# Performance work log

Measured on AMD Instinct MI355X. Metric: run time of the kernel, lower is better.

## Reference

```python
import jax, jax.numpy as jnp
import numpy as np

B, L, C, S, W, R = 2, 32, 32, 64, 64, 32
MH = 32  # forcing MLP hidden


def _conv3d(x, w, b, pad_hw):
    # x: [B, Cin, L, S, W], w: [Cout, Cin, 1, kh, kw]
    y = jax.lax.conv_general_dilated(
        x, w, window_strides=(1, 1, 1),
        padding=[(0, 0), (pad_hw, pad_hw), (pad_hw, pad_hw)],
        dimension_numbers=('NCDHW', 'OIDHW', 'NCDHW'))
    return y + b[None, :, None, None, None]


def _forward(x, listT, params_log_base, dispersion_mod, fm_W1, fm_b1, fm_W2, fm_b2,
             forcing_scale, U_re, U_im, V_re, V_im, pW_re, pW_im, pb_re, pb_im,
             convr_w, convr_b, convi_w, convi_b, projc_w, projc_b, ln_w, ln_b):
    b, l, c, s, w = x.shape
    r = U_re.shape[-1]
    pad = s // 4
    dt = listT.reshape(b, l, 1, 1, 1)

    # FFT with mirror padding along S
    xp = jnp.pad(x, ((0, 0), (0, 0), (0, 0), (pad, pad), (0, 0)), mode='reflect')
    h = jnp.fft.fft2(xp.astype(jnp.complex64), axes=(-2, -1), norm='ortho')

    # complex channel projection
    proj_W = pW_re + 1j * pW_im
    h = jnp.einsum('blcsw,cd->bldsw', h, proj_W)
    h = h + (pb_re + 1j * pb_im)[None, None, :, None, None]

    # back to spatial, crop pad, re-FFT
    hs = jnp.fft.ifft2(h, axes=(-2, -1), norm='ortho')[..., pad:-pad, :]
    h = jnp.fft.fft2(hs, axes=(-2, -1), norm='ortho')

    U = U_re + 1j * U_im          # [C, S, R]
    V = V_re + 1j * V_im          # [C, W, R]
    # zq[b,l,c,r,q] = sum_{s,w} h * conj(U)[c,s,r] * V[c,w,q]
    zq = jnp.einsum('blcsw,csr,cwq->blcrq', h, jnp.conj(U), V)

    nu_base = jnp.exp(params_log_base[0] + dispersion_mod[0]).reshape(1, 1, c, r, 1)
    th_base = jnp.exp(params_log_base[1] + dispersion_mod[1]).reshape(1, 1, c, r, 1)

    # forcing modulation
    ctx = x.mean(axis=(-2, -1))                       # [B, L, C]
    inp = jnp.concatenate([ctx, dt.reshape(b, l, 1)], axis=-1)
    mid = jnp.tanh(inp @ fm_W1 + fm_b1)
    mod = (mid @ fm_W2 + fm_b2).reshape(b, l, c, r, 2)
    dnu = (forcing_scale * jnp.tanh(mod[..., 0]))[..., None]
    dth = (forcing_scale * jnp.tanh(mod[..., 1]))[..., None]

    nu_t = jnp.maximum(nu_base * dt + dnu, 1e-6)       # [B, L, C, R, 1]
    th_t = th_base * dt + dth
    lamb = jnp.exp(jax.lax.complex(-nu_t, th_t))       # complex [B, L, C, R, 1]

    gamma = jnp.sqrt(jnp.maximum(1.0 - jnp.exp(-2.0 * nu_t), 1e-12))
    x_in = zq * gamma.astype(zq.dtype)                 # [B, L, C, R, R]

    # parallel linear-recurrence scan: z_t = lamb_t * z_{t-1} + x_t
    def comb(a, bb):
        a1, x1 = a
        a2, x2 = bb
        return a1 * a2, a2 * x1 + x2
    _, z_out = jax.lax.associative_scan(comb, (lamb, x_in), axis=1)

    # reconstruct spectral field and inverse FFT
    h_rec = jnp.einsum('blcrq,cwq,csr->blcsw', z_out, jnp.conj(V), U)
    h_sp = jnp.fft.ifft2(h_rec, axes=(-2, -1), norm='ortho')

    xr = jnp.transpose(h_sp.real, (0, 2, 1, 3, 4))     # [B, C, L, S, W]
    xi = jnp.transpose(h_sp.imag, (0, 2, 1, 3, 4))
    hr = _conv3d(xr, convr_w, convr_b, 1)
    hi = _conv3d(xi, convi_w, convi_b, 1)
    hf = _conv3d(jnp.concatenate([hr, hi], axis=1), projc_w, projc_b, 0)
    hf = jnp.transpose(hf, (0, 2, 1, 3, 4))            # [B, L, C, S, W]

    # LayerNorm over [S, W]
    mu = hf.mean(axis=(-2, -1), keepdims=True)
    var = hf.var(axis=(-2, -1), keepdims=True)
    hf = (hf - mu) / jnp.sqrt(var + 1e-5) * ln_w + ln_b

    return x + hf


def setup_inputs() -> dict:
    key = jax.random.key(0)
    ks = jax.random.split(key, 20)
    f32 = jnp.float32
    x = jax.random.normal(ks[0], (B, L, C, S, W), dtype=f32)
    listT = jax.random.uniform(ks[1], (B, L), dtype=f32, minval=0.5, maxval=1.5)

    r_min, r_max = 0.8, 0.99
    u1 = jax.random.uniform(ks[2], (C, R), dtype=f32)
    u2 = jax.random.uniform(ks[3], (C, R), dtype=f32)
    nu_log = jnp.log(-0.5 * jnp.log(u1 * (r_max ** 2 - r_min ** 2) + r_min ** 2))
    theta_log = jnp.log(u2 * (2.0 * np.pi))
    params_log_base = jnp.stack([nu_log, theta_log], axis=0)
    dispersion_mod = jnp.zeros((2, C, R), dtype=f32)

    fm_W1 = jax.random.normal(ks[4], (C + 1, MH), dtype=f32) / np.sqrt(C + 1)
    fm_b1 = jnp.zeros((MH,), dtype=f32)
    fm_W2 = jax.random.normal(ks[5], (MH, C * R * 2), dtype=f32) / np.sqrt(MH)
    fm_b2 = jnp.zeros((C * R * 2,), dtype=f32)
    forcing_scale = jnp.float32(0.1)

    cplx_scale = 1.0 / np.sqrt(2.0)
    U_re = jax.random.normal(ks[6], (C, S, R), dtype=f32) * cplx_scale / np.sqrt(S)
    U_im = jax.random.normal(ks[7], (C, S, R), dtype=f32) * cplx_scale / np.sqrt(S)
    V_re = jax.random.normal(ks[8], (C, W, R), dtype=f32) * cplx_scale / np.sqrt(W)
    V_im = jax.random.normal(ks[9], (C, W, R), dtype=f32) * cplx_scale / np.sqrt(W)
    pW_re = jax.random.normal(ks[10], (C, C), dtype=f32) * cplx_scale / np.sqrt(C)
    pW_im = jax.random.normal(ks[11], (C, C), dtype=f32) * cplx_scale / np.sqrt(C)
    pb_re = jnp.zeros((C,), dtype=f32)
    pb_im = jnp.zeros((C,), dtype=f32)

    convr_w = jax.random.normal(ks[12], (C, C, 1, 3, 3), dtype=f32) * (1.0 / np.sqrt(C * 9))
    convr_b = jnp.zeros((C,), dtype=f32)
    convi_w = jax.random.normal(ks[13], (C, C, 1, 3, 3), dtype=f32) * (1.0 / np.sqrt(C * 9))
    convi_b = jnp.zeros((C,), dtype=f32)
    projc_w = jax.random.normal(ks[14], (C, 2 * C, 1, 1, 1), dtype=f32) * (1.0 / np.sqrt(2 * C))
    projc_b = jnp.zeros((C,), dtype=f32)

    ln_w = jnp.ones((S, W), dtype=f32)
    ln_b = jnp.zeros((S, W), dtype=f32)

    return dict(x=x, listT=listT, params_log_base=params_log_base,
                dispersion_mod=dispersion_mod, fm_W1=fm_W1, fm_b1=fm_b1,
                fm_W2=fm_W2, fm_b2=fm_b2, forcing_scale=forcing_scale,
                U_re=U_re, U_im=U_im, V_re=V_re, V_im=V_im,
                pW_re=pW_re, pW_im=pW_im, pb_re=pb_re, pb_im=pb_im,
                convr_w=convr_w, convr_b=convr_b, convi_w=convi_w, convi_b=convi_b,
                projc_w=projc_w, projc_b=projc_b, ln_w=ln_w, ln_b=ln_b)


def reference(x, listT, params_log_base, dispersion_mod, fm_W1, fm_b1, fm_W2, fm_b2,
              forcing_scale, U_re, U_im, V_re, V_im, pW_re, pW_im, pb_re, pb_im,
              convr_w, convr_b, convi_w, convi_b, projc_w, projc_b, ln_w, ln_b):
    return _forward(x, listT, params_log_base, dispersion_mod, fm_W1, fm_b1, fm_W2,
                    fm_b2, forcing_scale, U_re, U_im, V_re, V_im, pW_re, pW_im,
                    pb_re, pb_im, convr_w, convr_b, convi_w, convi_b, projc_w,
                    projc_b, ln_w, ln_b)
```

## Files before the change

### kernel.cpp

```cpp
#include <hip/hip_runtime.h>


typedef __attribute__((ext_vector_type(8))) short short8;
typedef __attribute__((ext_vector_type(4))) float floatx4;

__device__ __forceinline__ unsigned pack_bf16(float re, float im) {
  unsigned a = __float_as_uint(re), b = __float_as_uint(im);
  a = (a + 0x7FFFu + ((a >> 16) & 1u)) >> 16;
  b = (b + 0x7FFFu + ((b >> 16) & 1u)) >> 16;
  return a | (b << 16);
}
__device__ __forceinline__ unsigned short bf16r(float v) {
  unsigned a = __float_as_uint(v);
  return (unsigned short)((a + 0x7FFFu + ((a >> 16) & 1u)) >> 16);
}

__global__ __launch_bounds__(256) void k_mixprep(
    const float* __restrict__ x, const float* __restrict__ pWr,
    const float* __restrict__ pWi,
    const float* __restrict__ U_re, const float* __restrict__ U_im,
    const float* __restrict__ V_re, const float* __restrict__ V_im,
    const float* __restrict__ projc_w, const float* __restrict__ convr_w,
    const float* __restrict__ convi_w,
    unsigned* __restrict__ hs, float* __restrict__ ctxp,
    unsigned* __restrict__ zqA, unsigned* __restrict__ recA,
    unsigned* __restrict__ recB, unsigned* __restrict__ Wtb) {
  __shared__ __align__(16) char smem[33280];
  const int tid = threadIdx.x;
  if (blockIdx.x < 1024) {
    unsigned* xb_s = (unsigned*)smem;
    float(*red)[16][2] = (float(*)[16][2])(smem + 20480);
    unsigned* outb = (unsigned*)smem;
    const int bl = blockIdx.x >> 4;
    const int seg = blockIdx.x & 15;
    const int pxbase = seg * 256;
    const float* xb = x + (size_t)bl * 131072 + pxbase;
    float csa = 0.f, csb = 0.f;
#pragma unroll
    for (int t = 0; t < 4; ++t) {
      int i = t * 256 + tid;
      int c2 = i & 15, g4 = i >> 4;
      float4 a = *(const float4*)(xb + (2 * c2) * 4096 + g4 * 4);
      float4 b = *(const float4*)(xb + (2 * c2 + 1) * 4096 + g4 * 4);
      csa += a.x + a.y + a.z + a.w;
      csb += b.x + b.y + b.z + b.w;
#pragma unroll
      for (int j = 0; j < 4; ++j) {
        int px = g4 * 4 + j;
        xb_s[px * 20 + (((c2 >> 2) ^ (px & 3)) << 2) + (c2 & 3)] =
            pack_bf16(((const float*)&a)[j], ((const float*)&b)[j]);
      }
    }
    red[tid & 15][tid >> 4][0] = csa;
    red[tid & 15][tid >> 4][1] = csb;
    const int lane = tid & 63, wv = tid >> 6;
    const int qd = lane >> 4, ln = lane & 15;
    short8 arL, aiL, arH, aiH;
#pragma unroll
    for (int j = 0; j < 8; ++j) {
      int ci = qd * 8 + j;
      ((short*)&arL)[j] = (short)bf16r(pWr[ci * 32 + ln]);
      ((short*)&aiL)[j] = (short)bf16r(pWi[ci * 32 + ln]);
      ((short*)&arH)[j] = (short)bf16r(pWr[ci * 32 + 16 + ln]);
      ((short*)&aiH)[j] = (short)bf16r(pWi[ci * 32 + 16 + ln]);
    }
    __syncthreads();
    if (tid < 32) {
      int c2 = tid >> 1, part = tid & 1;
      float s = 0.f;
#pragma unroll
      for (int w = 0; w < 16; ++w) s += red[c2][w][part];
      ctxp[(bl * 16 + seg) * 32 + 2 * c2 + part] = s;
    }
    floatx4 RL[4], IL[4], RH[4], IH[4];
#pragma unroll
    for (int pt = 0; pt < 4; ++pt) {
      int pxt = wv * 4 + pt;
      int pxl = pxt * 16 + ln;
      short8 bfr = *(const short8*)&xb_s[pxl * 20 + ((qd ^ (pxl & 3)) << 2)];
      floatx4 z4 = {0.f, 0.f, 0.f, 0.f};
      RL[pt] = __builtin_amdgcn_mfma_f32_16x16x32_bf16(arL, bfr, z4, 0, 0, 0);
      IL[pt] = __builtin_amdgcn_mfma_f32_16x16x32_bf16(aiL, bfr, z4, 0, 0, 0);
      RH[pt] = __builtin_amdgcn_mfma_f32_16x16x32_bf16(arH, bfr, z4, 0, 0, 0);
      IH[pt] = __builtin_amdgcn_mfma_f32_16x16x32_bf16(aiH, bfr, z4, 0, 0, 0);
    }
    __syncthreads();
#pragma unroll
    for (int pt = 0; pt < 4; ++pt) {
      int px = (wv * 4 + pt) * 16 + ln;
#pragma unroll
      for (int j = 0; j < 4; ++j) {
        outb[(qd * 4 + j) * 260 + px] = pack_bf16(RL[pt][j], IL[pt][j]);
        outb[(16 + qd * 4 + j) * 260 + px] = pack_bf16(RH[pt][j], IH[pt][j]);
      }
    }
    __syncthreads();
    unsigned* ho = hs + (size_t)bl * 131072 + pxbase;
    const int px4 = tid & 63, dg = tid >> 6;
#pragma unroll
    for (int dd = 0; dd < 8; ++dd) {
      int d = dg * 8 + dd;
      uint4 v = *(const uint4*)&outb[d * 260 + px4 * 4];
      *(uint4*)(ho + d * 4096 + px4 * 4) = v;
    }
  } else if (blockIdx.x < 1088) {
    float2* A2 = (float2*)smem;
    float2* tw = (float2*)(smem + 16384);
    const int id = blockIdx.x - 1024;
    const int c = id >> 1, src = id & 1;
    const float* Ar = (src ? V_re : U_re) + c * 2048;
    const float* Ai = (src ? V_im : U_im) + c * 2048;
    if (tid < 64) {
      float sa, ca;
      sincosf((float)tid * 0.09817477042468103f, &sa, &ca);
      tw[tid] = make_float2(ca, sa);
    }
#pragma unroll
    for (int t = 0; t < 8; ++t) {
      int idx = t * 256 + tid;
      A2[idx] = make_float2(Ar[idx], Ai[idx]);
    }
    __syncthreads();
    const int kw = tid >> 2, mg = tid & 3;
    float sr[8] = {0.f, 0.f, 0.f, 0.f, 0.f, 0.f, 0.f, 0.f};
    float si[8] = {0.f, 0.f, 0.f, 0.f, 0.f, 0.f, 0.f, 0.f};
#pragma unroll 4
    for (int n = 0; n < 64; ++n) {
      float2 w = tw[(kw * n) & 63];
      float ws = src ? -w.y : w.y;
#pragma unroll
      for (int t4 = 0; t4 < 4; ++t4) {
        float4 p = *(const float4*)&A2[n * 32 + mg * 8 + t4 * 2];
        sr[2 * t4]     += p.x * w.x - p.y * ws;
        si[2 * t4]     += p.x * ws + p.y * w.x;
        sr[2 * t4 + 1] += p.z * w.x - p.w * ws;
        si[2 * t4 + 1] += p.z * ws + p.w * w.x;
      }
    }
#pragma unroll
    for (int j = 0; j < 8; ++j) {
      float r = sr[j] * 0.125f, i2 = si[j] * 0.125f;
      int m = mg * 8 + j;
      unsigned p_ri  = pack_bf16(r, i2);
      unsigned p_rmi = pack_bf16(r, -i2);
      unsigned p_ir  = pack_bf16(i2, r);
      unsigned p_mir = pack_bf16(-i2, r);
      if (src == 0) {
        zqA[((c * 4 + 2) * 32 + m) * 64 + kw] = p_ri;
        zqA[((c * 4 + 3) * 32 + m) * 64 + kw] = p_mir;
        recA[((c * 2 + 0) * 64 + kw) * 32 + m] = p_rmi;
        recA[((c * 2 + 1) * 64 + kw) * 32 + m] = p_ir;
      } else {
        zqA[((c * 4 + 0) * 32 + m) * 64 + kw] = p_rmi;
        zqA[((c * 4 + 1) * 32 + m) * 64 + kw] = p_ir;
        recB[((c * 2 + 0) * 64 + kw) * 32 + m] = p_ri;
        recB[((c * 2 + 1) * 64 + kw) * 32 + m] = p_mir;
      }
    }
  } else {
    int gid = (blockIdx.x - 1088) * 256 + tid;
    if (gid < 9216) {
      int co = gid / 288;
      int r2 = gid - co * 288;
      int tap = r2 >> 5, ci = r2 & 31;
      float sr = 0.f, si = 0.f;
      for (int m = 0; m < 32; ++m) {
        sr += projc_w[co * 64 + m]      * convr_w[(m * 32 + ci) * 9 + tap];
        si += projc_w[co * 64 + 32 + m] * convi_w[(m * 32 + ci) * 9 + tap];
      }
      Wtb[gid] = pack_bf16(sr, si);
    }
  }
}

__global__ __launch_bounds__(256) void k_zq(
    const unsigned* __restrict__ hs, const short* __restrict__ zqA,
    float2* __restrict__ zq,
    const float* __restrict__ ctxp, const float* __restrict__ listT,
    const float* __restrict__ plb, const float* __restrict__ dmod,
    const float* __restrict__ W1, const float* __restrict__ b1,
    const float* __restrict__ W2, const float* __restrict__ b2,
    const float* __restrict__ fscale,
    float2* __restrict__ lam, float* __restrict__ gam) {
  __shared__ unsigned HsB[4096];
  __shared__ unsigned T2[2048];
  __shared__ float mid_s[32];
  __shared__ float ctxs[32];
  const int tid = threadIdx.x;
  if (blockIdx.x >= 2048) {
    int bl = blockIdx.x - 2048;
    float dt = listT[bl];
    if (tid < 32) {
      float s = 0.f;
#pragma unroll
      for (int sg = 0; sg < 16; ++sg) s += ctxp[(bl * 16 + sg) * 32 + tid];
      ctxs[tid] = s * (1.f / 4096.f);
    }
    __syncthreads();
    if (tid < 32) {
      float a = b1[tid];
      for (int j = 0; j < 32; ++j) a += ctxs[j] * W1[j * 32 + tid];
      a += dt * W1[1024 + tid];
      mid_s[tid] = tanhf(a);
    }
    __syncthreads();
    float fs = fscale[0];
#pragma unroll
    for (int u = 0; u < 4; ++u) {
      int cr = u * 256 + tid;
      int col = cr * 2;
      float m0 = b2[col], m1 = b2[col + 1];
      for (int h = 0; h < 32; ++h) {
        float mh = mid_s[h];
        float2 w2 = *(const float2*)&W2[h * 2048 + col];
        m0 += mh * w2.x;
        m1 += mh * w2.y;
      }
      float dnu = fs * tanhf(m0);
      float dth = fs * tanhf(m1);
      float nub = expf(plb[cr] + dmod[cr]);
      float thb = expf(plb[1024 + cr] + dmod[1024 + cr]);
      float nut = fmaxf(nub * dt + dnu, 1e-6f);
      float tht = thb * dt + dth;
      float e = expf(-nut);
      float sa, ca;
      sincosf(tht, &sa, &ca);
      float g = sqrtf(fmaxf(1.f - expf(-2.f * nut), 1e-12f));
      int o = bl * 1024 + cr;
      lam[o] = make_float2(e * ca, e * sa);
      gam[o] = g;
    }
    return;
  }
  const int blc = blockIdx.x;
  const int c = blc & 31;
  const int lane = tid & 63, wv = tid >> 6;
  const int qd = lane >> 4, ln = lane & 15;
  const int mt = wv >> 1, nth = wv & 1;
  {
    const uint4* hp = (const uint4*)(hs + (size_t)blc * 4096);
#pragma unroll
    for (int it = 0; it < 4; ++it) {
      int i4 = tid + it * 256;
      uint4 v = hp[i4];
      int s = i4 >> 4, w4 = i4 & 15;
      *(uint4*)&HsB[s * 64 + ((w4 ^ (s & 15)) << 2)] = v;
    }
  }
  const short* zA = zqA + (size_t)c * 4 * 32 * 128;
  short8 a1[4], a2[4], a3[4], a4[4];
#pragma unroll
  for (int t = 0; t < 4; ++t) {
    int row = mt * 16 + ln;
    a1[t] = *(const short8*)(zA + (0 * 32 + row) * 128 + t * 32 + qd * 8);
    a2[t] = *(const short8*)(zA + (1 * 32 + row) * 128 + t * 32 + qd * 8);
    a3[t] = *(const short8*)(zA + (2 * 32 + row) * 128 + t * 32 + qd * 8);
    a4[t] = *(const short8*)(zA + (3 * 32 + row) * 128 + t * 32 + qd * 8);
  }
  __syncthreads();
#pragma unroll
  for (int nti = 0; nti < 2; ++nti) {
    int nt = nth * 2 + nti;
    int n = nt * 16 + ln;
    floatx4 accr = {0.f, 0.f, 0.f, 0.f}, acci = {0.f, 0.f, 0.f, 0.f};
#pragma unroll
    for (int t = 0; t < 4; ++t) {
      short8 b = *(const short8*)&HsB[n * 64 + (((4 * t + qd) ^ (n & 15)) << 2)];
      accr = __builtin_amdgcn_mfma_f32_16x16x32_bf16(a1[t], b, accr, 0, 0, 0);
      acci = __builtin_amdgcn_mfma_f32_16x16x32_bf16(a2[t], b, acci, 0, 0, 0);
    }
#pragma unroll
    for (int j = 0; j < 4; ++j) {
      int q = mt * 16 + qd * 4 + j;
      int s = n;
      T2[q * 64 + (((s >> 2) ^ (q & 15)) << 2) + (s & 3)] = pack_bf16(accr[j], acci[j]);
    }
  }
  __syncthreads();
  {
    const int mt2 = wv >> 1, nt2 = wv & 1;
    int n = nt2 * 16 + ln;
    floatx4 zr = {0.f, 0.f, 0.f, 0.f}, zi = {0.f, 0.f, 0.f, 0.f};
#pragma unroll
    for (int t = 0; t < 4; ++t) {
      short8 b = *(const short8*)&T2[n * 64 + (((4 * t + qd) ^ (n & 15)) << 2)];
      zr = __builtin_amdgcn_mfma_f32_16x16x32_bf16(a3[t], b, zr, 0, 0, 0);
      zi = __builtin_amdgcn_mfma_f32_16x16x32_bf16(a4[t], b, zi, 0, 0, 0);
    }
    float2* zo = zq + (size_t)blc * 1024;
#pragma unroll
    for (int j = 0; j < 4; ++j) {
      int r = mt2 * 16 + qd * 4 + j;
      zo[r * 32 + n] = make_float2(zr[j], zi[j]);
    }
  }
}

__global__ __launch_bounds__(256) void k_scan(const float2* __restrict__ lam,
                                              const float* __restrict__ gam,
                                              const float2* __restrict__ zin,
                                              unsigned* __restrict__ zsp,
                                              int zst) {
  __shared__ float2 se[4][64];
  __shared__ float2 pe[4][64];
  __shared__ float2 cr_s[4][64];
  const int bc = blockIdx.x >> 4;
  const int b = bc >> 5, c = bc & 31;
  const int rq0 = (blockIdx.x & 15) * 64;
  const int seg = threadIdx.x >> 6, u = threadIdx.x & 63;
  const int rq = rq0 + u, r = rq >> 5;
  const int t0 = seg * 8;
  float2 s = make_float2(0.f, 0.f), P = make_float2(1.f, 0.f);
  float2 zloc[8], Ps[8];
  float2 v = zin[((size_t)(b * 32 + t0) * 32 + c) * 1024 + rq];
  float2 lm = lam[(b * 32 + t0) * 1024 + c * 32 + r];
  float g = gam[(b * 32 + t0) * 1024 + c * 32 + r];
#pragma unroll
  for (int i = 0; i < 8; ++i) {
    float2 nv, nlm;
    float ng;
    if (i < 7) {
      int t = t0 + i + 1;
      nv = zin[((size_t)(b * 32 + t) * 32 + c) * 1024 + rq];
      nlm = lam[(b * 32 + t) * 1024 + c * 32 + r];
      ng = gam[(b * 32 + t) * 1024 + c * 32 + r];
    }
    float nr = lm.x * s.x - lm.y * s.y + g * v.x;
    float ni = lm.x * s.y + lm.y * s.x + g * v.y;
    s = make_float2(nr, ni);
    float pr = P.x * lm.x - P.y * lm.y;
    float pi = P.x * lm.y + P.y * lm.x;
    P = make_float2(pr, pi);
    zloc[i] = s;
    Ps[i] = P;
    v = nv; lm = nlm; g = ng;
  }
  se[seg][u] = s;
  pe[seg][u] = P;
  __syncthreads();
  if (threadIdx.x < 64) {
    float2 c1 = se[0][u];
    float2 p1 = pe[1][u], s1 = se[1][u];
    float2 c2 = make_float2(s1.x + p1.x * c1.x - p1.y * c1.y,
                            s1.y + p1.x * c1.y + p1.y * c1.x);
    float2 p2 = pe[2][u], s2 = se[2][u];
    float2 c3 = make_float2(s2.x + p2.x * c2.x - p2.y * c2.y,
                            s2.y + p2.x * c2.y + p2.y * c2.x);
    cr_s[0][u] = make_float2(0.f, 0.f);
    cr_s[1][u] = c1;
    cr_s[2][u] = c2;
    cr_s[3][u] = c3;
  }
  __syncthreads();
  float2 cr = cr_s[seg][u];
#pragma unroll
  for (int i = 0; i < 8; ++i) {
    float zr = zloc[i].x + Ps[i].x * cr.x - Ps[i].y * cr.y;
    float zi = zloc[i].y + Ps[i].x * cr.y + Ps[i].y * cr.x;
    size_t idx = ((size_t)(b * 32 + t0 + i) * 32 + c) * 1024 + rq;
    zsp[idx * zst] = pack_bf16(zr, zi);
  }
}

__global__ __launch_bounds__(256) void k_rec(const unsigned* __restrict__ zs,
                                             int zst,
                                             const short* __restrict__ recA,
                                             const short* __restrict__ recB,
                                             unsigned* __restrict__ hsp) {
  __shared__ unsigned zB[1024];
  __shared__ unsigned P[2048];
  const int blc = blockIdx.x;
  const int c = blc & 31;
  const int tid = threadIdx.x;
  const int lane = tid & 63, wv = tid >> 6;
  const int qd = lane >> 4, ln = lane & 15;
  {
    const unsigned* zp = zs + (size_t)blc * 1024 * zst;
#pragma unroll
    for (int it = 0; it < 4; ++it) {
      int i = tid + it * 256;
      unsigned pv = zp[(size_t)i * zst];
      int r = i >> 5, q = i & 31;
      zB[q * 32 + (((r >> 2) ^ (q & 7)) << 2) + (r & 3)] = pv;
    }
  }
  const short* rA = recA + (size_t)c * 2 * 64 * 64;
  short8 a5[2], a6[2];
#pragma unroll
  for (int t = 0; t < 2; ++t) {
    int row = wv * 16 + ln;
    a5[t] = *(const short8*)(rA + (0 * 64 + row) * 64 + t * 32 + qd * 8);
    a6[t] = *(const short8*)(rA + (1 * 64 + row) * 64 + t * 32 + qd * 8);
  }
  __syncthreads();
#pragma unroll
  for (int nt = 0; nt < 2; ++nt) {
    int n = nt * 16 + ln;
    floatx4 pr = {0.f, 0.f, 0.f, 0.f}, pi = {0.f, 0.f, 0.f, 0.f};
#pragma unroll
    for (int t = 0; t < 2; ++t) {
      short8 b = *(const short8*)&zB[n * 32 + (((4 * t + qd) ^ (n & 7)) << 2)];
      pr = __builtin_amdgcn_mfma_f32_16x16x32_bf16(a5[t], b, pr, 0, 0, 0);
      pi = __builtin_amdgcn_mfma_f32_16x16x32_bf16(a6[t], b, pi, 0, 0, 0);
    }
#pragma unroll
    for (int j = 0; j < 4; ++j) {
      int s = wv * 16 + qd * 4 + j;
      int q = n;
      P[s * 32 + (((q >> 2) ^ (s & 7)) << 2) + (q & 3)] = pack_bf16(pr[j], pi[j]);
    }
  }
  __syncthreads();
  const short* rB = recB + (size_t)c * 2 * 64 * 64;
  short8 pa[2];
#pragma unroll
  for (int t = 0; t < 2; ++t) {
    int row = wv * 16 + ln;
    pa[t] = *(const short8*)&P[row * 32 + (((4 * t + qd) ^ (row & 7)) << 2)];
  }
#pragma unroll
  for (int nt = 0; nt < 4; ++nt) {
    int n = nt * 16 + ln;
    floatx4 hr = {0.f, 0.f, 0.f, 0.f}, hi = {0.f, 0.f, 0.f, 0.f};
#pragma unroll
    for (int t = 0; t < 2; ++t) {
      short8 b5 = *(const short8*)(rB + (0 * 64 + n) * 64 + t * 32 + qd * 8);
      short8 b6 = *(const short8*)(rB + (1 * 64 + n) * 64 + t * 32 + qd * 8);
      hr = __builtin_amdgcn_mfma_f32_16x16x32_bf16(pa[t], b5, hr, 0, 0, 0);
      hi = __builtin_amdgcn_mfma_f32_16x16x32_bf16(pa[t], b6, hi, 0, 0, 0);
    }
    unsigned* ho = hsp + (size_t)blc * 4096;
#pragma unroll
    for (int j = 0; j < 4; ++j) {
      int s = wv * 16 + qd * 4 + j;
      ho[s * 64 + n] = pack_bf16(hr[j], hi[j]);
    }
  }
}

__global__ __launch_bounds__(256, 2) void k_conv(
    const unsigned* __restrict__ hsp, const short* __restrict__ Wtb,
    unsigned short* __restrict__ convout, float2* __restrict__ stats) {
  __shared__ unsigned lds_in[6 * 66 * 32];
  const int bl = blockIdx.x >> 4;
  const int slab = blockIdx.x & 15;
  const int y0 = slab * 4;
  const int tid = threadIdx.x;
  for (int i = tid; i < 384; i += 256) {
    int ci = i & 31, j = i >> 5;
    int yi = j >> 1, xi = (j & 1) ? 65 : 0;
    int slot = (ci >> 2) ^ (xi & 7);
    lds_in[(yi * 66 + xi) * 32 + slot * 4 + (ci & 3)] = 0u;
  }
#pragma unroll
  for (int t = 0; t < 12; ++t) {
    int i = t * 256 + tid;
    int ci = i & 31;
    int j = i >> 5;
    int yi = j >> 4, x4 = j & 15;
    int y = y0 + yi - 1;
    uint4 v = make_uint4(0u, 0u, 0u, 0u);
    if ((unsigned)y < 64u)
      v = *(const uint4*)(hsp + (((size_t)bl * 32 + ci) * 64 + y) * 64 + x4 * 4);
    int xb = 1 + x4 * 4;
#pragma unroll
    for (int jj = 0; jj < 4; ++jj) {
      int xi = xb + jj;
      int slot = (ci >> 2) ^ (xi & 7);
      lds_in[(yi * 66 + xi) * 32 + slot * 4 + (ci & 3)] =
          ((const unsigned*)&v)[jj];
    }
  }
  const int lane = tid & 63;
  const int wv = tid >> 6;
  const int co = lane & 15;
  const int qd = lane >> 4;
  short8 bL[18], bH[18];
  {
    const short* wpL = Wtb + (co * 9) * 64 + qd * 8;
    const short* wpH = Wtb + ((co + 16) * 9) * 64 + qd * 8;
#pragma unroll
    for (int tap = 0; tap < 9; ++tap)
#pragma unroll
      for (int kk = 0; kk < 2; ++kk) {
        bL[tap * 2 + kk] = *(const short8*)(wpL + tap * 64 + kk * 32);
        bH[tap * 2 + kk] = *(const short8*)(wpH + tap * 64 + kk * 32);
      }
  }
  __syncthreads();
  float sL = 0.f, s2L = 0.f, sH = 0.f, s2H = 0.f;
  const int x0 = wv * 16;
  const int xl = lane & 15;
  for (int ry = 0; ry < 4; ++ry) {
    floatx4 aL = {0.f, 0.f, 0.f, 0.f}, aH = {0.f, 0.f, 0.f, 0.f};
#pragma unroll
    for (int tap = 0; tap < 9; ++tap) {
      int dy = tap / 3, dx = tap - dy * 3;
      int yi = ry + dy;
      int xi = x0 + xl + dx;
#pragma unroll
      for (int kk = 0; kk < 2; ++kk) {
        int slot = ((kk << 2) | qd) ^ (xi & 7);
        const short8 a =
            *(const short8*)&lds_in[(yi * 66 + xi) * 32 + slot * 4];
        aL = __builtin_amdgcn_mfma_f32_16x16x32_bf16(a, bL[tap * 2 + kk], aL, 0, 0, 0);
        aH = __builtin_amdgcn_mfma_f32_16x16x32_bf16(a, bH[tap * 2 + kk], aH, 0, 0, 0);
      }
    }
    size_t goL = (((size_t)bl * 32 + co) * 64 + (y0 + ry)) * 64 + x0 + qd * 4;
    size_t goH = goL + (size_t)16 * 4096;
    *(uint2*)(convout + goL) =
        make_uint2(pack_bf16(aL[0], aL[1]), pack_bf16(aL[2], aL[3]));
    *(uint2*)(convout + goH) =
        make_uint2(pack_bf16(aH[0], aH[1]), pack_bf16(aH[2], aH[3]));
#pragma unroll
    for (int j = 0; j < 4; ++j) {
      sL += aL[j]; s2L += aL[j] * aL[j];
      sH += aH[j]; s2H += aH[j] * aH[j];
    }
  }
  sL += __shfl_down(sL, 32, 64);  s2L += __shfl_down(s2L, 32, 64);
  sH += __shfl_down(sH, 32, 64);  s2H += __shfl_down(s2H, 32, 64);
  sL += __shfl_down(sL, 16, 64);  s2L += __shfl_down(s2L, 16, 64);
  sH += __shfl_down(sH, 16, 64);  s2H += __shfl_down(s2H, 16, 64);
  if (lane < 16) {
    stats[((size_t)bl * 32 + lane) * 64 + slab * 4 + wv] = make_float2(sL, s2L);
    stats[((size_t)bl * 32 + 16 + lane) * 64 + slab * 4 + wv] =
        make_float2(sH, s2H);
  }
}

__global__ __launch_bounds__(256) void k_ln(
    const unsigned short* __restrict__ convout,
    const float2* __restrict__ stats, const float* __restrict__ x,
    const float* __restrict__ ln_w, const float* __restrict__ ln_b,
    float* __restrict__ out) {
  const int blc = blockIdx.x;
  const int tid = threadIdx.x;
  __shared__ float sh_mu, sh_rs;
  if (tid < 64) {
    float2 v = stats[(size_t)blc * 64 + tid];
    float s = v.x, s2 = v.y;
#pragma unroll
    for (int o = 32; o > 0; o >>= 1) {
      s += __shfl_down(s, o, 64);
      s2 += __shfl_down(s2, o, 64);
    }
    if (tid == 0) {
      float mu = s * (1.f / 4096.f);
      float var = s2 * (1.f / 4096.f) - mu * mu;
      sh_mu = mu;
      sh_rs = rsqrtf(var + 1e-5f);
    }
  }
  __syncthreads();
  float mu = sh_mu, rs = sh_rs;
  const uint2* cp = (const uint2*)(convout + (size_t)blc * 4096);
  const float4* xp = (const float4*)(x + (size_t)blc * 4096);
  const float4* lwp = (const float4*)ln_w;
  const float4* lbp = (const float4*)ln_b;
  float4* op = (float4*)(out + (size_t)blc * 4096);
#pragma unroll
  for (int k = 0; k < 4; ++k) {
    int i = tid + k * 256;
    uint2 cv = cp[i];
    float4 xv = xp[i], lw = lwp[i], lb = lbp[i];
    float c0 = __uint_as_float(cv.x << 16);
    float c1 = __uint_as_float(cv.x & 0xFFFF0000u);
    float c2 = __uint_as_float(cv.y << 16);
    float c3 = __uint_as_float(cv.y & 0xFFFF0000u);
    float4 o;
    o.x = xv.x + (c0 - mu) * rs * lw.x + lb.x;
    o.y = xv.y + (c1 - mu) * rs * lw.y + lb.y;
    o.z = xv.z + (c2 - mu) * rs * lw.z + lb.z;
    o.w = xv.w + (c3 - mu) * rs * lw.w + lb.w;
    op[i] = o;
  }
}

extern "C" void kernel_launch(void* const* d_in, const int* in_sizes, int n_in,
                              void* d_out, int out_size, void* d_ws,
                              size_t ws_size, hipStream_t stream) {
  const float* x       = (const float*)d_in[0];
  const float* listT   = (const float*)d_in[1];
  const float* plb     = (const float*)d_in[2];
  const float* dmod    = (const float*)d_in[3];
  const float* fm_W1   = (const float*)d_in[4];
  const float* fm_b1   = (const float*)d_in[5];
  const float* fm_W2   = (const float*)d_in[6];
  const float* fm_b2   = (const float*)d_in[7];
  const float* fscale  = (const float*)d_in[8];
  const float* U_re    = (const float*)d_in[9];
  const float* U_im    = (const float*)d_in[10];
  const float* V_re    = (const float*)d_in[11];
  const float* V_im    = (const float*)d_in[12];
  const float* pW_re   = (const float*)d_in[13];
  const float* pW_im   = (const float*)d_in[14];
  const float* convr_w = (const float*)d_in[17];
  const float* convi_w = (const float*)d_in[19];
  const float* projc_w = (const float*)d_in[21];
  const float* ln_w    = (const float*)d_in[23];
  const float* ln_b    = (const float*)d_in[24];
  float* out = (float*)d_out;

  float* wsf = (float*)d_ws;
  unsigned* hs  = (unsigned*)wsf;
  unsigned* hsp = (unsigned*)wsf;
  unsigned* zqAp  = (unsigned*)(wsf + 8388608);
  unsigned* recAp = (unsigned*)(wsf + 8388608 + 262144);
  unsigned* recBp = (unsigned*)(wsf + 8388608 + 393216);
  unsigned short* convout = (unsigned short*)(wsf + 8388608);
  float2*   stats = (float2*)(wsf + 12582912);
  float2*   zq  = (float2*)(wsf + 16777216);
  size_t off = 16777216 + 4194304;
  const size_t tail = 238592;
  unsigned* zs;
  int zst;
  size_t off2;
  if (ws_size >= (off + 2097152 + tail) * 4) {
    zs = (unsigned*)(wsf + off); zst = 1; off2 = off + 2097152;
  } else {
    zs = (unsigned*)zq; zst = 2; off2 = off;
  }
  float2*   lam  = (float2*)(wsf + off2);
  float*    gam  = wsf + off2 + 131072;
  float*    ctxp = wsf + off2 + 196608;
  unsigned* Wtb  = (unsigned*)(wsf + off2 + 229376);

  k_mixprep<<<1124, 256, 0, stream>>>(x, pW_re, pW_im, U_re, U_im, V_re, V_im,
                                      projc_w, convr_w, convi_w, hs, ctxp,
                                      zqAp, recAp, recBp, Wtb);
  k_zq<<<2112, 256, 0, stream>>>(hs, (const short*)zqAp, zq, ctxp, listT, plb,
                                 dmod, fm_W1, fm_b1, fm_W2, fm_b2, fscale,
                                 lam, gam);
  k_scan<<<1024, 256, 0, stream>>>(lam, gam, zq, zs, zst);
  k_rec<<<2048, 256, 0, stream>>>(zs, zst, (const short*)recAp,
                                  (const short*)recBp, hsp);
  k_conv<<<1024, 256, 0, stream>>>(hsp, (const short*)Wtb, convout, stats);
  k_ln<<<2048, 256, 0, stream>>>(convout, stats, x, ln_w, ln_b, out);
}
```

Before: 240.2 us.

## Split conv output channels across 512-thread blocks and hoist loads in scan and LN

The conv kernel now runs 8 waves per block, with each wave computing 16 output channels instead of 32. This halves the per-thread weight registers and doubles the number of waves available to hide latency. The scan kernel now issues all 8 timestep loads before the recurrence, and the LN kernel issues its global loads before the stats reduction and barrier so that memory latency overlaps. The trade-off is that each conv A-fragment read from LDS now feeds one MFMA instead of two, which doubles LDS read traffic per output.

```diff
diff --git a/kernel.cpp b/kernel.cpp
--- a/kernel.cpp
+++ b/kernel.cpp
@@ -310,30 +310,28 @@
   const int seg = threadIdx.x >> 6, u = threadIdx.x & 63;
   const int rq = rq0 + u, r = rq >> 5;
   const int t0 = seg * 8;
+  float2 vv[8], ll[8];
+  float gg[8];
+#pragma unroll
+  for (int i = 0; i < 8; ++i) {
+    int t = b * 32 + t0 + i;
+    vv[i] = zin[((size_t)t * 32 + c) * 1024 + rq];
+    ll[i] = lam[t * 1024 + c * 32 + r];
+    gg[i] = gam[t * 1024 + c * 32 + r];
+  }
   float2 s = make_float2(0.f, 0.f), P = make_float2(1.f, 0.f);
   float2 zloc[8], Ps[8];
-  float2 v = zin[((size_t)(b * 32 + t0) * 32 + c) * 1024 + rq];
-  float2 lm = lam[(b * 32 + t0) * 1024 + c * 32 + r];
-  float g = gam[(b * 32 + t0) * 1024 + c * 32 + r];
 #pragma unroll
   for (int i = 0; i < 8; ++i) {
-    float2 nv, nlm;
-    float ng;
-    if (i < 7) {
-      int t = t0 + i + 1;
-      nv = zin[((size_t)(b * 32 + t) * 32 + c) * 1024 + rq];
-      nlm = lam[(b * 32 + t) * 1024 + c * 32 + r];
-      ng = gam[(b * 32 + t) * 1024 + c * 32 + r];
-    }
-    float nr = lm.x * s.x - lm.y * s.y + g * v.x;
-    float ni = lm.x * s.y + lm.y * s.x + g * v.y;
+    float2 lm = ll[i];
+    float nr = lm.x * s.x - lm.y * s.y + gg[i] * vv[i].x;
+    float ni = lm.x * s.y + lm.y * s.x + gg[i] * vv[i].y;
     s = make_float2(nr, ni);
     float pr = P.x * lm.x - P.y * lm.y;
     float pi = P.x * lm.y + P.y * lm.x;
     P = make_float2(pr, pi);
     zloc[i] = s;
     Ps[i] = P;
-    v = nv; lm = nlm; g = ng;
   }
   se[seg][u] = s;
   pe[seg][u] = P;
@@ -438,7 +436,7 @@
   }
 }
 
-__global__ __launch_bounds__(256, 2) void k_conv(
+__global__ __launch_bounds__(512, 4) void k_conv(
     const unsigned* __restrict__ hsp, const short* __restrict__ Wtb,
     unsigned short* __restrict__ convout, float2* __restrict__ stats) {
   __shared__ unsigned lds_in[6 * 66 * 32];
@@ -446,15 +444,15 @@
   const int slab = blockIdx.x & 15;
   const int y0 = slab * 4;
   const int tid = threadIdx.x;
-  for (int i = tid; i < 384; i += 256) {
-    int ci = i & 31, j = i >> 5;
+  if (tid < 384) {
+    int ci = tid & 31, j = tid >> 5;
     int yi = j >> 1, xi = (j & 1) ? 65 : 0;
     int slot = (ci >> 2) ^ (xi & 7);
     lds_in[(yi * 66 + xi) * 32 + slot * 4 + (ci & 3)] = 0u;
   }
 #pragma unroll
-  for (int t = 0; t < 12; ++t) {
-    int i = t * 256 + tid;
+  for (int t = 0; t < 6; ++t) {
+    int i = t * 512 + tid;
     int ci = i & 31;
     int j = i >> 5;
     int yi = j >> 4, x4 = j & 15;
@@ -473,26 +471,24 @@
   }
   const int lane = tid & 63;
   const int wv = tid >> 6;
+  const int quarter = wv & 3, cog = wv >> 2;
   const int co = lane & 15;
   const int qd = lane >> 4;
-  short8 bL[18], bH[18];
+  short8 bW[18];
   {
-    const short* wpL = Wtb + (co * 9) * 64 + qd * 8;
-    const short* wpH = Wtb + ((co + 16) * 9) * 64 + qd * 8;
+    const short* wp = Wtb + ((cog * 16 + co) * 9) * 64 + qd * 8;
 #pragma unroll
     for (int tap = 0; tap < 9; ++tap)
 #pragma unroll
-      for (int kk = 0; kk < 2; ++kk) {
-        bL[tap * 2 + kk] = *(const short8*)(wpL + tap * 64 + kk * 32);
-        bH[tap * 2 + kk] = *(const short8*)(wpH + tap * 64 + kk * 32);
-      }
-  }
-  __syncthreads();
-  float sL = 0.f, s2L = 0.f, sH = 0.f, s2H = 0.f;
-  const int x0 = wv * 16;
+      for (int kk = 0; kk < 2; ++kk)
+        bW[tap * 2 + kk] = *(const short8*)(wp + tap * 64 + kk * 32);
+  }
+  __syncthreads();
+  float sA = 0.f, s2A = 0.f;
+  const int x0 = quarter * 16;
   const int xl = lane & 15;
   for (int ry = 0; ry < 4; ++ry) {
-    floatx4 aL = {0.f, 0.f, 0.f, 0.f}, aH = {0.f, 0.f, 0.f, 0.f};
+    floatx4 acc = {0.f, 0.f, 0.f, 0.f};
 #pragma unroll
     for (int tap = 0; tap < 9; ++tap) {
       int dy = tap / 3, dx = tap - dy * 3;
@@ -503,30 +499,23 @@
         int slot = ((kk << 2) | qd) ^ (xi & 7);
         const short8 a =
             *(const short8*)&lds_in[(yi * 66 + xi) * 32 + slot * 4];
-        aL = __builtin_amdgcn_mfma_f32_16x16x32_bf16(a, bL[tap * 2 + kk], aL, 0, 0, 0);
-        aH = __builtin_amdgcn_mfma_f32_16x16x32_bf16(a, bH[tap * 2 + kk], aH, 0, 0, 0);
+        acc = __builtin_amdgcn_mfma_f32_16x16x32_bf16(a, bW[tap * 2 + kk], acc, 0, 0, 0);
       }
     }
-    size_t goL = (((size_t)bl * 32 + co) * 64 + (y0 + ry)) * 64 + x0 + qd * 4;
-    size_t goH = goL + (size_t)16 * 4096;
-    *(uint2*)(convout + goL) =
-        make_uint2(pack_bf16(aL[0], aL[1]), pack_bf16(aL[2], aL[3]));
-    *(uint2*)(convout + goH) =
-        make_uint2(pack_bf16(aH[0], aH[1]), pack_bf16(aH[2], aH[3]));
+    size_t go =
+        (((size_t)bl * 32 + cog * 16 + co) * 64 + (y0 + ry)) * 64 + x0 + qd * 4;
+    *(uint2*)(convout + go) =
+        make_uint2(pack_bf16(acc[0], acc[1]), pack_bf16(acc[2], acc[3]));
 #pragma unroll
     for (int j = 0; j < 4; ++j) {
-      sL += aL[j]; s2L += aL[j] * aL[j];
-      sH += aH[j]; s2H += aH[j] * aH[j];
-    }
-  }
-  sL += __shfl_down(sL, 32, 64);  s2L += __shfl_down(s2L, 32, 64);
-  sH += __shfl_down(sH, 32, 64);  s2H += __shfl_down(s2H, 32, 64);
-  sL += __shfl_down(sL, 16, 64);  s2L += __shfl_down(s2L, 16, 64);
-  sH += __shfl_down(sH, 16, 64);  s2H += __shfl_down(s2H, 16, 64);
+      sA += acc[j]; s2A += acc[j] * acc[j];
+    }
+  }
+  sA += __shfl_down(sA, 32, 64);  s2A += __shfl_down(s2A, 32, 64);
+  sA += __shfl_down(sA, 16, 64);  s2A += __shfl_down(s2A, 16, 64);
   if (lane < 16) {
-    stats[((size_t)bl * 32 + lane) * 64 + slab * 4 + wv] = make_float2(sL, s2L);
-    stats[((size_t)bl * 32 + 16 + lane) * 64 + slab * 4 + wv] =
-        make_float2(sH, s2H);
+    stats[((size_t)bl * 32 + cog * 16 + lane) * 64 + slab * 4 + quarter] =
+        make_float2(sA, s2A);
   }
 }
 
@@ -538,6 +527,21 @@
   const int blc = blockIdx.x;
   const int tid = threadIdx.x;
   __shared__ float sh_mu, sh_rs;
+  const uint2* cp = (const uint2*)(convout + (size_t)blc * 4096);
+  const float4* xp = (const float4*)(x + (size_t)blc * 4096);
+  const float4* lwp = (const float4*)ln_w;
+  const float4* lbp = (const float4*)ln_b;
+  float4* op = (float4*)(out + (size_t)blc * 4096);
+  uint2 cv[4];
+  float4 xv[4], lw[4], lb[4];
+#pragma unroll
+  for (int k = 0; k < 4; ++k) {
+    int i = tid + k * 256;
+    cv[k] = cp[i];
+    xv[k] = xp[i];
+    lw[k] = lwp[i];
+    lb[k] = lbp[i];
+  }
   if (tid < 64) {
     float2 v = stats[(size_t)blc * 64 + tid];
     float s = v.x, s2 = v.y;
@@ -555,25 +559,18 @@
   }
   __syncthreads();
   float mu = sh_mu, rs = sh_rs;
-  const uint2* cp = (const uint2*)(convout + (size_t)blc * 4096);
-  const float4* xp = (const float4*)(x + (size_t)blc * 4096);
-  const float4* lwp = (const float4*)ln_w;
-  const float4* lbp = (const float4*)ln_b;
-  float4* op = (float4*)(out + (size_t)blc * 4096);
 #pragma unroll
   for (int k = 0; k < 4; ++k) {
     int i = tid + k * 256;
-    uint2 cv = cp[i];
-    float4 xv = xp[i], lw = lwp[i], lb = lbp[i];
-    float c0 = __uint_as_float(cv.x << 16);
-    float c1 = __uint_as_float(cv.x & 0xFFFF0000u);
-    float c2 = __uint_as_float(cv.y << 16);
-    float c3 = __uint_as_float(cv.y & 0xFFFF0000u);
+    float c0 = __uint_as_float(cv[k].x << 16);
+    float c1 = __uint_as_float(cv[k].x & 0xFFFF0000u);
+    float c2 = __uint_as_float(cv[k].y << 16);
+    float c3 = __uint_as_float(cv[k].y & 0xFFFF0000u);
     float4 o;
-    o.x = xv.x + (c0 - mu) * rs * lw.x + lb.x;
-    o.y = xv.y + (c1 - mu) * rs * lw.y + lb.y;
-    o.z = xv.z + (c2 - mu) * rs * lw.z + lb.z;
-    o.w = xv.w + (c3 - mu) * rs * lw.w + lb.w;
+    o.x = xv[k].x + (c0 - mu) * rs * lw[k].x + lb[k].x;
+    o.y = xv[k].y + (c1 - mu) * rs * lw[k].y + lb[k].y;
+    o.z = xv[k].z + (c2 - mu) * rs * lw[k].z + lb[k].z;
+    o.w = xv[k].w + (c3 - mu) * rs * lw[k].w + lb[k].w;
     op[i] = o;
   }
 }
@@ -636,6 +633,6 @@
   k_scan<<<1024, 256, 0, stream>>>(lam, gam, zq, zs, zst);
   k_rec<<<2048, 256, 0, stream>>>(zs, zst, (const short*)recAp,
                                   (const short*)recBp, hsp);
-  k_conv<<<1024, 256, 0, stream>>>(hsp, (const short*)Wtb, convout, stats);
+  k_conv<<<1024, 512, 0, stream>>>(hsp, (const short*)Wtb, convout, stats);
   k_ln<<<2048, 256, 0, stream>>>(convout, stats, x, ln_w, ln_b, out);
 }
```

Result: no change. 242.2 us (+0.8%).
